# Optimization experiments

Measured on AMD Instinct MI355X. Metric: run time of the kernel, lower is better.

Reference implementation:

```python
import jax, jax.numpy as jnp
import numpy as np

NC = 100000   # n cells
NG = 8000     # n genes
D = 128       # h_dim
E_CG, E_GC, E_CC, E_GG = 1500000, 1500000, 1000000, 200000
SLOPE = 0.05  # LeakyReLU negative slope
LN_EPS = 1e-5


def setup_inputs() -> dict:
    key = jax.random.key(0)
    ks = jax.random.split(key, 16)
    f32 = jnp.float32
    inp = {
        "h_cell": jax.random.normal(ks[0], (NC, D), f32),
        "h_gene": jax.random.normal(ks[1], (NG, D), f32),
        "src_cg": jax.random.randint(ks[2], (E_CG,), 0, NC),
        "dst_cg": jax.random.randint(ks[3], (E_CG,), 0, NG),
        "src_gc": jax.random.randint(ks[4], (E_GC,), 0, NG),
        "dst_gc": jax.random.randint(ks[5], (E_GC,), 0, NC),
        "src_cc": jax.random.randint(ks[6], (E_CC,), 0, NC),
        "dst_cc": jax.random.randint(ks[7], (E_CC,), 0, NC),
        "src_gg": jax.random.randint(ks[8], (E_GG,), 0, NG),
        "dst_gg": jax.random.randint(ks[9], (E_GG,), 0, NG),
        "W_cg": jax.random.normal(ks[10], (D, D), f32) * (1.0 / np.sqrt(D)),
        "W_gc": jax.random.normal(ks[11], (D, D), f32) * (1.0 / np.sqrt(D)),
        "W_cc": jax.random.normal(ks[12], (D, D), f32) * (1.0 / np.sqrt(D)),
        "W_gg": jax.random.normal(ks[13], (D, D), f32) * (1.0 / np.sqrt(D)),
        "b_cell": jnp.zeros((D,), f32),
        "b_gene": jnp.zeros((D,), f32),
        "ln_s_cell": jnp.ones((D,), f32),
        "ln_b_cell": jnp.zeros((D,), f32),
        "ln_s_gene": jnp.ones((D,), f32),
        "ln_b_gene": jnp.zeros((D,), f32),
    }
    return inp


def _rel_conv(h_src, W, src, dst, n_dst):
    # per-relation GraphConv, norm='right': transform, gather, scatter-sum, / in-degree
    m = (h_src @ W)[src]                                   # [E, D]
    agg = jax.ops.segment_sum(m, dst, num_segments=n_dst)  # [n_dst, D]
    deg = jax.ops.segment_sum(jnp.ones(dst.shape, m.dtype), dst, num_segments=n_dst)
    return agg / jnp.clip(deg, 1.0)[:, None]


def _layernorm(x, s, b):
    mu = jnp.mean(x, axis=-1, keepdims=True)
    var = jnp.var(x, axis=-1, keepdims=True)
    return (x - mu) * jax.lax.rsqrt(var + LN_EPS) * s + b


def _leaky(x):
    return jnp.where(x >= 0, x, SLOPE * x)


def _shared_layer(hc, hg, idx, p):
    # aggregate='sum' over relations targeting each dst ntype, then bias, act, LN
    oc = (_rel_conv(hg, p["W_gc"], idx["src_gc"], idx["dst_gc"], NC)
          + _rel_conv(hc, p["W_cc"], idx["src_cc"], idx["dst_cc"], NC)
          + p["b_cell"])
    og = (_rel_conv(hc, p["W_cg"], idx["src_cg"], idx["dst_cg"], NG)
          + _rel_conv(hg, p["W_gg"], idx["src_gg"], idx["dst_gg"], NG)
          + p["b_gene"])
    oc = _layernorm(_leaky(oc), p["ln_s_cell"], p["ln_b_cell"])
    og = _layernorm(_leaky(og), p["ln_s_gene"], p["ln_b_gene"])
    return oc, og


def reference(h_cell, h_gene, src_cg, dst_cg, src_gc, dst_gc, src_cc, dst_cc,
              src_gg, dst_gg, W_cg, W_gc, W_cc, W_gg, b_cell, b_gene,
              ln_s_cell, ln_b_cell, ln_s_gene, ln_b_gene):
    idx = dict(src_cg=src_cg, dst_cg=dst_cg, src_gc=src_gc, dst_gc=dst_gc,
               src_cc=src_cc, dst_cc=dst_cc, src_gg=src_gg, dst_gg=dst_gg)
    p = dict(W_cg=W_cg, W_gc=W_gc, W_cc=W_cc, W_gg=W_gg,
             b_cell=b_cell, b_gene=b_gene,
             ln_s_cell=ln_s_cell, ln_b_cell=ln_b_cell,
             ln_s_gene=ln_s_gene, ln_b_gene=ln_b_gene)
    hc, hg = h_cell, h_gene
    for _ in range(2):  # num_hidden_layers=2, SAME shared layer both times
        hc, hg = _shared_layer(hc, hg, idx, p)
    # pack the heterogeneous output dict as one array: [NC+NG, D]
    return jnp.concatenate([hc, hg], axis=0)
```

## Files before the change

### kernel.cpp

```cpp
#include <hip/hip_runtime.h>

#define NCELL 100000
#define NGENE 8000
#define DIM   128
#define NE_CG 1500000
#define NE_GC 1500000
#define NE_CC 1000000
#define NE_GG 200000
#define SLOPE 0.05f
#define LN_EPS 1e-5f

typedef __attribute__((ext_vector_type(2))) _Float16 f16x2;
typedef __attribute__((ext_vector_type(8))) _Float16 f16x8;
typedef __attribute__((ext_vector_type(4))) float f32x4;

__device__ __forceinline__ unsigned short f2h(float x) {
    return __builtin_bit_cast(unsigned short, (_Float16)x);
}
__device__ __forceinline__ unsigned pack2h(float x, float y) {
    f16x2 h = { (_Float16)x, (_Float16)y };
    return __builtin_bit_cast(unsigned, h);
}
__device__ __forceinline__ f16x2 u2h2(unsigned u) {
    return __builtin_bit_cast(f16x2, u);
}

__global__ __launch_bounds__(256)
void conv2_k(const float* __restrict__ inc, unsigned short* __restrict__ outc,
             const float* __restrict__ ing, unsigned short* __restrict__ outg,
             int cellBlocks, int n2c, int n2g) {
    const float* in; unsigned short* out; int i, n2;
    if ((int)blockIdx.x < cellBlocks) {
        in = inc; out = outc; n2 = n2c; i = blockIdx.x * 256 + threadIdx.x;
    } else {
        in = ing; out = outg; n2 = n2g; i = (blockIdx.x - cellBlocks) * 256 + threadIdx.x;
    }
    if (i < n2) {
        float2 v = ((const float2*)in)[i];
        ((unsigned*)out)[i] = pack2h(v.x, v.y);
    }
}

__global__ void pack2_w_k(const float* __restrict__ WAc, const float* __restrict__ WBc,
                          unsigned short* __restrict__ Wpc,
                          const float* __restrict__ WAg, const float* __restrict__ WBg,
                          unsigned short* __restrict__ Wpg) {
    int bb = blockIdx.x;
    const float *WA, *WB; unsigned short* Wp;
    if (bb < 64) { WA = WAc; WB = WBc; Wp = Wpc; }
    else { bb -= 64; WA = WAg; WB = WBg; Wp = Wpg; }
    int lane = threadIdx.x;
    int t = bb >> 3, c = bb & 7;
    int n = t * 16 + (lane & 15);
    int k0 = c * 32 + (lane >> 4) * 8;
    #pragma unroll
    for (int j = 0; j < 8; ++j) {
        int k = k0 + j;
        float x = (k < 128) ? WA[k * 128 + n] : WB[(k - 128) * 128 + n];
        Wp[((size_t)(bb * 64 + lane)) * 8 + j] = f2h(x);
    }
}

struct RelP {
    const int* src; const int* dst; int n; int shift;
    int nbins; int N; int cap;
    int* deg; int* offg; int* bkt;
    int* bcur; unsigned* stg;
    int cblk0;
    int sblk0;
};

__global__ __launch_bounds__(256)
void bin_fill4_k(RelP r0, RelP r1, RelP r2, RelP r3) {
    int b = blockIdx.x;
    RelP R = (b >= r3.cblk0) ? r3 : (b >= r2.cblk0) ? r2 : (b >= r1.cblk0) ? r1 : r0;
    int lb = b - R.cblk0;
    __shared__ int cnt[512];
    __shared__ int basem[512];
    int tid = threadIdx.x;
    cnt[tid] = 0; cnt[tid + 256] = 0;
    __syncthreads();
    int base = lb * 4096;
    int bins[16]; int ranks[16]; unsigned pk[16];
    #pragma unroll
    for (int it = 0; it < 16; ++it) {
        int i = base + it * 256 + tid;
        bins[it] = -1;
        if (i < R.n) {
            int d = R.dst[i];
            int bn = d >> R.shift;
            int dl = d & ((1 << R.shift) - 1);
            bins[it] = bn;
            pk[it] = (unsigned)R.src[i] | ((unsigned)dl << 20);
            ranks[it] = atomicAdd(&cnt[bn], 1);
        }
    }
    __syncthreads();
    if (cnt[tid])       basem[tid]       = atomicAdd(&R.bcur[tid],       cnt[tid]);
    if (cnt[tid + 256]) basem[tid + 256] = atomicAdd(&R.bcur[tid + 256], cnt[tid + 256]);
    __syncthreads();
    #pragma unroll
    for (int it = 0; it < 16; ++it)
        if (bins[it] >= 0) {
            int r = basem[bins[it]] + ranks[it];
            if (r >= R.cap) r = R.cap - 1;
            R.stg[(size_t)bins[it] * R.cap + r] = pk[it];
        }
}

__global__ __launch_bounds__(256)
void bin_csr4_k(RelP r0, RelP r1, RelP r2, RelP r3) {
    int b = blockIdx.x;
    RelP R = (b >= r3.sblk0) ? r3 : (b >= r2.sblk0) ? r2 : (b >= r1.sblk0) ? r1 : r0;
    int lb = b - R.sblk0;
    int tid = threadIdx.x;
    int ebase = lb * R.cap;
    int cnt = R.bcur[lb]; if (cnt > R.cap) cnt = R.cap;
    __shared__ int degm[256];
    __shared__ int sc[256];
    __shared__ int cur[256];
    __shared__ int bktl[4352];
    degm[tid] = 0;
    __syncthreads();
    for (int i = tid; i < cnt; i += 256)
        atomicAdd(&degm[(R.stg[ebase + i] >> 20) & 255], 1);
    __syncthreads();
    int x = degm[tid];
    sc[tid] = x;
    __syncthreads();
    for (int ofs = 1; ofs < 256; ofs <<= 1) {
        int t = (tid >= ofs) ? sc[tid - ofs] : 0;
        __syncthreads();
        sc[tid] += t;
        __syncthreads();
    }
    int excl = sc[tid] - x;
    cur[tid] = excl;
    int node = (lb << R.shift) + tid;
    if (tid < (1 << R.shift) && node < R.N) { R.deg[node] = x; R.offg[node] = ebase + excl; }
    __syncthreads();
    for (int i = tid; i < cnt; i += 256) {
        unsigned p = R.stg[ebase + i];
        int dl = (p >> 20) & 255;
        int r = atomicAdd(&cur[dl], 1);
        bktl[r] = (int)(p & 0xFFFFFu);
    }
    __syncthreads();
    for (int i = tid; i < cnt; i += 256)
        R.bkt[ebase + i] = bktl[i];
}

__global__ __launch_bounds__(256)
void gather2_k(const unsigned short* __restrict__ hc, const unsigned short* __restrict__ hg,
               const int* __restrict__ off_gc, const int* __restrict__ deg_gc, const int* __restrict__ bkt_gc,
               const int* __restrict__ off_cc, const int* __restrict__ deg_cc, const int* __restrict__ bkt_cc,
               const int* __restrict__ off_cg, const int* __restrict__ deg_cg, const int* __restrict__ bkt_cg,
               const int* __restrict__ off_gg, const int* __restrict__ deg_gg, const int* __restrict__ bkt_gg,
               unsigned short* __restrict__ Acat_c, unsigned short* __restrict__ Acat_g,
               int geneBlocks) {
    int wave = threadIdx.x >> 6, lane = threadIdx.x & 63;
    int g = lane >> 4, c = lane & 15;
    const unsigned short *hA, *hB;
    const int *offA, *degA, *bktA, *offB, *degB, *bktB;
    unsigned short* Aout; int node, N;
    if ((int)blockIdx.x < geneBlocks) {
        node = blockIdx.x * 4 + wave; N = NGENE;
        hA = hc; offA = off_cg; degA = deg_cg; bktA = bkt_cg;
        hB = hg; offB = off_gg; degB = deg_gg; bktB = bkt_gg;
        Aout = Acat_g;
    } else {
        node = (blockIdx.x - geneBlocks) * 4 + wave; N = NCELL;
        hA = hg; offA = off_gc; degA = deg_gc; bktA = bkt_gc;
        hB = hc; offB = off_cc; degB = deg_cc; bktB = bkt_cc;
        Aout = Acat_c;
    }
    if (node >= N) return;

    int nA = degA[node], sA = offA[node];
    int nB = degB[node], sB = offB[node];

    f16x2 aA[4], aB[4];
    #pragma unroll
    for (int i = 0; i < 4; ++i) { aA[i] = (f16x2)(_Float16)0; aB[i] = (f16x2)(_Float16)0; }
    int mx = (nA > nB) ? nA : nB;

    for (int j0 = 0; j0 < mx; j0 += 32) {
        int l32 = lane & 31;
        int jj = j0 + l32;
        int iv = 0;
        if (lane < 32) { if (jj < nA) iv = bktA[sA + jj]; }
        else           { if (jj < nB) iv = bktB[sB + jj]; }
        int mA = nA - j0;
        int mB = nB - j0;
        #pragma unroll
        for (int t = 0; t < 8; ++t) {
            int j = t * 4 + g;
            int sidxA = __shfl(iv, j);
            int sidxB = __shfl(iv, 32 + j);
            uint4 vA = *(const uint4*)(hA + (size_t)sidxA * DIM + c * 8);
            uint4 vB = *(const uint4*)(hB + (size_t)sidxB * DIM + c * 8);
            if (j < mA) {
                aA[0] += u2h2(vA.x); aA[1] += u2h2(vA.y);
                aA[2] += u2h2(vA.z); aA[3] += u2h2(vA.w);
            }
            if (j < mB) {
                aB[0] += u2h2(vB.x); aB[1] += u2h2(vB.y);
                aB[2] += u2h2(vB.z); aB[3] += u2h2(vB.w);
            }
        }
    }

    float fA[8], fB[8];
    #pragma unroll
    for (int i = 0; i < 4; ++i) {
        fA[2 * i]     = (float)aA[i][0]; fA[2 * i + 1] = (float)aA[i][1];
        fB[2 * i]     = (float)aB[i][0]; fB[2 * i + 1] = (float)aB[i][1];
    }
    #pragma unroll
    for (int i = 0; i < 8; ++i) {
        fA[i] += __shfl_xor(fA[i], 16); fA[i] += __shfl_xor(fA[i], 32);
        fB[i] += __shfl_xor(fB[i], 16); fB[i] += __shfl_xor(fB[i], 32);
    }
    float invA = 1.0f / fmaxf((float)nA, 1.0f);
    float invB = 1.0f / fmaxf((float)nB, 1.0f);
    uint4* outrow = (uint4*)(Aout + (size_t)node * 256);
    if (g == 0) {
        outrow[c] = make_uint4(pack2h(fA[0] * invA, fA[1] * invA), pack2h(fA[2] * invA, fA[3] * invA),
                               pack2h(fA[4] * invA, fA[5] * invA), pack2h(fA[6] * invA, fA[7] * invA));
    } else if (g == 1) {
        outrow[16 + c] = make_uint4(pack2h(fB[0] * invB, fB[1] * invB), pack2h(fB[2] * invB, fB[3] * invB),
                                    pack2h(fB[4] * invB, fB[5] * invB), pack2h(fB[6] * invB, fB[7] * invB));
    }
}

#define GBM 128
__global__ __launch_bounds__(256, 4)
void gemm2_ln_k(const unsigned short* __restrict__ Acat_c, const unsigned short* __restrict__ Acat_g,
                const unsigned short* __restrict__ Wp_c, const unsigned short* __restrict__ Wp_g,
                const float* __restrict__ bias_c, const float* __restrict__ bias_g,
                const float* __restrict__ ls_c, const float* __restrict__ lb_c,
                const float* __restrict__ ls_g, const float* __restrict__ lb_g,
                unsigned short* __restrict__ outh_c, unsigned short* __restrict__ outh_g,
                float* __restrict__ outf_c, float* __restrict__ outf_g,
                int cellBlocks) {
    const unsigned short *A, *Wp; const float *bias, *lns, *lnb;
    unsigned short* outh; float* outf; int M, mb;
    if ((int)blockIdx.x < cellBlocks) {
        A = Acat_c; Wp = Wp_c; bias = bias_c; lns = ls_c; lnb = lb_c;
        outh = outh_c; outf = outf_c; M = NCELL; mb = blockIdx.x;
    } else {
        A = Acat_g; Wp = Wp_g; bias = bias_g; lns = ls_g; lnb = lb_g;
        outh = outh_g; outf = outf_g; M = NGENE; mb = blockIdx.x - cellBlocks;
    }
    int tid = threadIdx.x;
    int wave = tid >> 6, lane = tid & 63;
    int col0 = lane & 15;
    int kq = lane >> 4;
    int m_base = mb * GBM + wave * 32;

    f32x4 acc[2][8];
    #pragma unroll
    for (int mt = 0; mt < 2; ++mt)
        #pragma unroll
        for (int t = 0; t < 8; ++t) acc[mt][t] = (f32x4){0.f, 0.f, 0.f, 0.f};

    const unsigned short* Ar0 = A + (size_t)(m_base + col0) * 256 + kq * 8;
    const unsigned short* Ar1 = Ar0 + 16 * 256;
    #pragma unroll
    for (int cc = 0; cc < 8; ++cc) {
        f16x8 a0 = *(const f16x8*)(Ar0 + cc * 32);
        f16x8 a1 = *(const f16x8*)(Ar1 + cc * 32);
        #pragma unroll
        for (int t = 0; t < 8; ++t) {
            f16x8 b = *(const f16x8*)(Wp + ((t * 8 + cc) * 64 + lane) * 8);
            acc[0][t] = __builtin_amdgcn_mfma_f32_16x16x32_f16(a0, b, acc[0][t], 0, 0, 0);
            acc[1][t] = __builtin_amdgcn_mfma_f32_16x16x32_f16(a1, b, acc[1][t], 0, 0, 0);
        }
    }

    float bias_r[8], s_r[8], b_r[8];
    #pragma unroll
    for (int t = 0; t < 8; ++t) {
        int col = t * 16 + col0;
        bias_r[t] = bias[col]; s_r[t] = lns[col]; b_r[t] = lnb[col];
    }
    #pragma unroll
    for (int mt = 0; mt < 2; ++mt) {
        #pragma unroll
        for (int r = 0; r < 4; ++r) {
            int row = m_base + mt * 16 + kq * 4 + r;
            float v[8]; float sum = 0.f, sq = 0.f;
            #pragma unroll
            for (int t = 0; t < 8; ++t) {
                float x = acc[mt][t][r] + bias_r[t];
                x = (x >= 0.f) ? x : SLOPE * x;
                v[t] = x; sum += x; sq += x * x;
            }
            #pragma unroll
            for (int ofs = 1; ofs <= 8; ofs <<= 1) {
                sum += __shfl_xor(sum, ofs);
                sq  += __shfl_xor(sq, ofs);
            }
            float mu = sum * (1.0f / 128.0f);
            float var = sq * (1.0f / 128.0f) - mu * mu;
            float rstd = rsqrtf(var + LN_EPS);
            if (row < M) {
                if (outh) {
                    #pragma unroll
                    for (int t = 0; t < 8; ++t)
                        outh[(size_t)row * 128 + t * 16 + col0] =
                            f2h((v[t] - mu) * rstd * s_r[t] + b_r[t]);
                } else {
                    #pragma unroll
                    for (int t = 0; t < 8; ++t)
                        outf[(size_t)row * 128 + t * 16 + col0] =
                            (v[t] - mu) * rstd * s_r[t] + b_r[t];
                }
            }
        }
    }
}

extern "C" void kernel_launch(void* const* d_in, const int* in_sizes, int n_in,
                              void* d_out, int out_size, void* d_ws, size_t ws_size,
                              hipStream_t stream) {
    const float* h_cell = (const float*)d_in[0];
    const float* h_gene = (const float*)d_in[1];
    const int* src_cg = (const int*)d_in[2];
    const int* dst_cg = (const int*)d_in[3];
    const int* src_gc = (const int*)d_in[4];
    const int* dst_gc = (const int*)d_in[5];
    const int* src_cc = (const int*)d_in[6];
    const int* dst_cc = (const int*)d_in[7];
    const int* src_gg = (const int*)d_in[8];
    const int* dst_gg = (const int*)d_in[9];
    const float* W_cg = (const float*)d_in[10];
    const float* W_gc = (const float*)d_in[11];
    const float* W_cc = (const float*)d_in[12];
    const float* W_gg = (const float*)d_in[13];
    const float* b_cell = (const float*)d_in[14];
    const float* b_gene = (const float*)d_in[15];
    const float* ln_s_cell = (const float*)d_in[16];
    const float* ln_b_cell = (const float*)d_in[17];
    const float* ln_s_gene = (const float*)d_in[18];
    const float* ln_b_gene = (const float*)d_in[19];
    float* out = (float*)d_out;

    const int MPC = ((NCELL + GBM - 1) / GBM) * GBM;
    const int MPG = ((NGENE + GBM - 1) / GBM) * GBM;
    const int NB_C = (NCELL + 255) / 256;
    const int NB_G = (NGENE + 15) / 16;
    const int CAP_GC = 4352;
    const int CAP_CC = 3072;
    const int CAP_CG = 3584;
    const int CAP_GG = 768;

    char* wsb = (char*)d_ws;
    size_t off = 0;
    auto alloc = [&](size_t bytes) -> char* {
        char* p = wsb + off;
        off = (off + bytes + 255) & ~(size_t)255;
        return p;
    };
    unsigned short* Acat_c = (unsigned short*)alloc((size_t)MPC * 256 * 2);
    unsigned short* Acat_g = (unsigned short*)alloc((size_t)MPG * 256 * 2);
    unsigned short* hcb0 = (unsigned short*)alloc((size_t)NCELL * DIM * 2);
    unsigned short* hgb0 = (unsigned short*)alloc((size_t)NGENE * DIM * 2);
    unsigned short* hcb1 = (unsigned short*)alloc((size_t)NCELL * DIM * 2);
    unsigned short* hgb1 = (unsigned short*)alloc((size_t)NGENE * DIM * 2);
    unsigned short* Wp_cell = (unsigned short*)alloc(65536);
    unsigned short* Wp_gene = (unsigned short*)alloc(65536);
    int ndeg = 2 * NCELL + 2 * NGENE;
    int* degs = (int*)alloc((size_t)ndeg * 4);
    int* deg_gc = degs;
    int* deg_cc = degs + NCELL;
    int* deg_cg = degs + 2 * NCELL;
    int* deg_gg = degs + 2 * NCELL + NGENE;
    int* offs = (int*)alloc((size_t)ndeg * 4);
    int* off_gc = offs;
    int* off_cc = offs + NCELL;
    int* off_cg = offs + 2 * NCELL;
    int* off_gg = offs + 2 * NCELL + NGENE;
    int* bkt_gc = (int*)alloc((size_t)NB_C * CAP_GC * 4);
    int* bkt_cc = (int*)alloc((size_t)NB_C * CAP_CC * 4);
    int* bkt_cg = (int*)alloc((size_t)NB_G * CAP_CG * 4);
    int* bkt_gg = (int*)alloc((size_t)NB_G * CAP_GG * 4);
    unsigned* stg_gc = (unsigned*)alloc((size_t)NB_C * CAP_GC * 4);
    unsigned* stg_cc = (unsigned*)alloc((size_t)NB_C * CAP_CC * 4);
    unsigned* stg_cg = (unsigned*)alloc((size_t)NB_G * CAP_CG * 4);
    unsigned* stg_gg = (unsigned*)alloc((size_t)NB_G * CAP_GG * 4);
    int* binmem = (int*)alloc(4 * 512 * 4);

    const int n2c = NCELL * DIM / 2, n2g = NGENE * DIM / 2;
    const int convCB = (n2c + 255) / 256;
    const int convGB = (n2g + 255) / 256;
    conv2_k<<<convCB + convGB, 256, 0, stream>>>(h_cell, hcb0, h_gene, hgb0, convCB, n2c, n2g);
    pack2_w_k<<<128, 64, 0, stream>>>(W_gc, W_cc, Wp_cell, W_cg, W_gg, Wp_gene);

    hipMemsetAsync(binmem, 0, 4 * 512 * 4, stream);
    const int nbk_gc = (NE_GC + 4095) / 4096;
    const int nbk_cc = (NE_CC + 4095) / 4096;
    const int nbk_cg = (NE_CG + 4095) / 4096;
    const int nbk_gg = (NE_GG + 4095) / 4096;
    auto mkrel = [&](const int* s, const int* d, int n, int shift, int nbins, int N, int cap,
                     int* deg, int* offg, int* bkt, int* bm, unsigned* stg,
                     int cblk0, int sblk0) {
        RelP r;
        r.src = s; r.dst = d; r.n = n; r.shift = shift; r.nbins = nbins; r.N = N; r.cap = cap;
        r.deg = deg; r.offg = offg; r.bkt = bkt;
        r.bcur = bm; r.stg = stg;
        r.cblk0 = cblk0; r.sblk0 = sblk0;
        return r;
    };
    RelP r0 = mkrel(src_gc, dst_gc, NE_GC, 8, NB_C, NCELL, CAP_GC, deg_gc, off_gc, bkt_gc,
                    binmem + 0 * 512, stg_gc, 0, 0);
    RelP r1 = mkrel(src_cc, dst_cc, NE_CC, 8, NB_C, NCELL, CAP_CC, deg_cc, off_cc, bkt_cc,
                    binmem + 1 * 512, stg_cc, nbk_gc, NB_C);
    RelP r2 = mkrel(src_cg, dst_cg, NE_CG, 4, NB_G, NGENE, CAP_CG, deg_cg, off_cg, bkt_cg,
                    binmem + 2 * 512, stg_cg, nbk_gc + nbk_cc, 2 * NB_C);
    RelP r3 = mkrel(src_gg, dst_gg, NE_GG, 4, NB_G, NGENE, CAP_GG, deg_gg, off_gg, bkt_gg,
                    binmem + 3 * 512, stg_gg, nbk_gc + nbk_cc + nbk_cg, 2 * NB_C + NB_G);
    const int cntBlocks = nbk_gc + nbk_cc + nbk_cg + nbk_gg;
    const int csrBlocks = 2 * NB_C + 2 * NB_G;
    bin_fill4_k<<<cntBlocks, 256, 0, stream>>>(r0, r1, r2, r3);
    bin_csr4_k<<<csrBlocks, 256, 0, stream>>>(r0, r1, r2, r3);

    const int gatherCB = NCELL / 4;
    const int gatherGB = (NGENE + 3) / 4;
    const int gemmCB = MPC / GBM;
    const int gemmGB = MPG / GBM;
    const unsigned short* hc = hcb0;
    const unsigned short* hg = hgb0;
    for (int layer = 0; layer < 2; ++layer) {
        int final_ = (layer == 1);
        gather2_k<<<gatherGB + gatherCB, 256, 0, stream>>>(
            hc, hg,
            off_gc, deg_gc, bkt_gc, off_cc, deg_cc, bkt_cc,
            off_cg, deg_cg, bkt_cg, off_gg, deg_gg, bkt_gg,
            Acat_c, Acat_g, gatherGB);
        gemm2_ln_k<<<gemmCB + gemmGB, 256, 0, stream>>>(
            Acat_c, Acat_g, Wp_cell, Wp_gene, b_cell, b_gene,
            ln_s_cell, ln_b_cell, ln_s_gene, ln_b_gene,
            final_ ? nullptr : hcb1, final_ ? nullptr : hgb1,
            final_ ? out : nullptr, final_ ? out + (size_t)NCELL * DIM : nullptr,
            gemmCB);
        hc = hcb1;
        hg = hgb1;
    }
}
```

Measured before the change: 563.6 us.

## Fuse input conversion and weight packing into bin-fill kernel; mask gather tail

Merges the fp32-to-fp16 feature conversion and weight packing kernels into the edge bin-fill kernel as extra block ranges, cutting two launches and letting the independent work overlap. The gather loop now skips sub-iterations beyond the larger of the two neighbor counts and replaces branchy conditional accumulation with bitmasked adds. This trades slightly larger kernel code and shared-memory allocation for conversion blocks in exchange for fewer launches and less divergence.

```diff
diff --git a/kernel.cpp b/kernel.cpp
--- a/kernel.cpp
+++ b/kernel.cpp
@@ -25,42 +25,6 @@
     return __builtin_bit_cast(f16x2, u);
 }
 
-__global__ __launch_bounds__(256)
-void conv2_k(const float* __restrict__ inc, unsigned short* __restrict__ outc,
-             const float* __restrict__ ing, unsigned short* __restrict__ outg,
-             int cellBlocks, int n2c, int n2g) {
-    const float* in; unsigned short* out; int i, n2;
-    if ((int)blockIdx.x < cellBlocks) {
-        in = inc; out = outc; n2 = n2c; i = blockIdx.x * 256 + threadIdx.x;
-    } else {
-        in = ing; out = outg; n2 = n2g; i = (blockIdx.x - cellBlocks) * 256 + threadIdx.x;
-    }
-    if (i < n2) {
-        float2 v = ((const float2*)in)[i];
-        ((unsigned*)out)[i] = pack2h(v.x, v.y);
-    }
-}
-
-__global__ void pack2_w_k(const float* __restrict__ WAc, const float* __restrict__ WBc,
-                          unsigned short* __restrict__ Wpc,
-                          const float* __restrict__ WAg, const float* __restrict__ WBg,
-                          unsigned short* __restrict__ Wpg) {
-    int bb = blockIdx.x;
-    const float *WA, *WB; unsigned short* Wp;
-    if (bb < 64) { WA = WAc; WB = WBc; Wp = Wpc; }
-    else { bb -= 64; WA = WAg; WB = WBg; Wp = Wpg; }
-    int lane = threadIdx.x;
-    int t = bb >> 3, c = bb & 7;
-    int n = t * 16 + (lane & 15);
-    int k0 = c * 32 + (lane >> 4) * 8;
-    #pragma unroll
-    for (int j = 0; j < 8; ++j) {
-        int k = k0 + j;
-        float x = (k < 128) ? WA[k * 128 + n] : WB[(k - 128) * 128 + n];
-        Wp[((size_t)(bb * 64 + lane)) * 8 + j] = f2h(x);
-    }
-}
-
 struct RelP {
     const int* src; const int* dst; int n; int shift;
     int nbins; int N; int cap;
@@ -71,13 +35,50 @@
 };
 
 __global__ __launch_bounds__(256)
-void bin_fill4_k(RelP r0, RelP r1, RelP r2, RelP r3) {
+void pre_k(RelP r0, RelP r1, RelP r2, RelP r3, int packBase, int convBase, int convCB,
+           const float* __restrict__ h_cell, unsigned short* __restrict__ hcb,
+           const float* __restrict__ h_gene, unsigned short* __restrict__ hgb,
+           int n2c, int n2g,
+           const float* __restrict__ WAc, const float* __restrict__ WBc,
+           unsigned short* __restrict__ Wpc,
+           const float* __restrict__ WAg, const float* __restrict__ WBg,
+           unsigned short* __restrict__ Wpg) {
+    __shared__ int cnt[512];
+    __shared__ int basem[512];
     int b = blockIdx.x;
+    int tid = threadIdx.x;
+
+    if (b >= convBase) {
+        int cb = b - convBase;
+        const float* in; unsigned short* out; int i, n2;
+        if (cb < convCB) { in = h_cell; out = hcb; n2 = n2c; i = cb * 256 + tid; }
+        else             { in = h_gene; out = hgb; n2 = n2g; i = (cb - convCB) * 256 + tid; }
+        if (i < n2) {
+            float2 v = ((const float2*)in)[i];
+            ((unsigned*)out)[i] = pack2h(v.x, v.y);
+        }
+        return;
+    }
+    if (b >= packBase) {
+        int sub = (b - packBase) * 4 + (tid >> 6);
+        int lane = tid & 63;
+        const float *WA, *WB; unsigned short* Wp; int bb;
+        if (sub < 64) { WA = WAc; WB = WBc; Wp = Wpc; bb = sub; }
+        else          { WA = WAg; WB = WBg; Wp = Wpg; bb = sub - 64; }
+        int t = bb >> 3, cc = bb & 7;
+        int n = t * 16 + (lane & 15);
+        int k0 = cc * 32 + (lane >> 4) * 8;
+        #pragma unroll
+        for (int j = 0; j < 8; ++j) {
+            int k = k0 + j;
+            float x = (k < 128) ? WA[k * 128 + n] : WB[(k - 128) * 128 + n];
+            Wp[((size_t)(bb * 64 + lane)) * 8 + j] = f2h(x);
+        }
+        return;
+    }
+
     RelP R = (b >= r3.cblk0) ? r3 : (b >= r2.cblk0) ? r2 : (b >= r1.cblk0) ? r1 : r0;
     int lb = b - R.cblk0;
-    __shared__ int cnt[512];
-    __shared__ int basem[512];
-    int tid = threadIdx.x;
     cnt[tid] = 0; cnt[tid + 256] = 0;
     __syncthreads();
     int base = lb * 4096;
@@ -192,20 +193,21 @@
         else           { if (jj < nB) iv = bktB[sB + jj]; }
         int mA = nA - j0;
         int mB = nB - j0;
+        int mxb = mx - j0;
         #pragma unroll
         for (int t = 0; t < 8; ++t) {
-            int j = t * 4 + g;
-            int sidxA = __shfl(iv, j);
-            int sidxB = __shfl(iv, 32 + j);
-            uint4 vA = *(const uint4*)(hA + (size_t)sidxA * DIM + c * 8);
-            uint4 vB = *(const uint4*)(hB + (size_t)sidxB * DIM + c * 8);
-            if (j < mA) {
-                aA[0] += u2h2(vA.x); aA[1] += u2h2(vA.y);
-                aA[2] += u2h2(vA.z); aA[3] += u2h2(vA.w);
-            }
-            if (j < mB) {
-                aB[0] += u2h2(vB.x); aB[1] += u2h2(vB.y);
-                aB[2] += u2h2(vB.z); aB[3] += u2h2(vB.w);
+            if (t * 4 < mxb) {
+                int j = t * 4 + g;
+                int sidxA = __shfl(iv, j);
+                int sidxB = __shfl(iv, 32 + j);
+                uint4 vA = *(const uint4*)(hA + (size_t)sidxA * DIM + c * 8);
+                uint4 vB = *(const uint4*)(hB + (size_t)sidxB * DIM + c * 8);
+                unsigned mskA = (j < mA) ? 0xFFFFFFFFu : 0u;
+                unsigned mskB = (j < mB) ? 0xFFFFFFFFu : 0u;
+                aA[0] += u2h2(vA.x & mskA); aA[1] += u2h2(vA.y & mskA);
+                aA[2] += u2h2(vA.z & mskA); aA[3] += u2h2(vA.w & mskA);
+                aB[0] += u2h2(vB.x & mskB); aB[1] += u2h2(vB.y & mskB);
+                aB[2] += u2h2(vB.z & mskB); aB[3] += u2h2(vB.w & mskB);
             }
         }
     }
@@ -391,12 +393,6 @@
     unsigned* stg_gg = (unsigned*)alloc((size_t)NB_G * CAP_GG * 4);
     int* binmem = (int*)alloc(4 * 512 * 4);
 
-    const int n2c = NCELL * DIM / 2, n2g = NGENE * DIM / 2;
-    const int convCB = (n2c + 255) / 256;
-    const int convGB = (n2g + 255) / 256;
-    conv2_k<<<convCB + convGB, 256, 0, stream>>>(h_cell, hcb0, h_gene, hgb0, convCB, n2c, n2g);
-    pack2_w_k<<<128, 64, 0, stream>>>(W_gc, W_cc, Wp_cell, W_cg, W_gg, Wp_gene);
-
     hipMemsetAsync(binmem, 0, 4 * 512 * 4, stream);
     const int nbk_gc = (NE_GC + 4095) / 4096;
     const int nbk_cc = (NE_CC + 4095) / 4096;
@@ -420,9 +416,18 @@
                     binmem + 2 * 512, stg_cg, nbk_gc + nbk_cc, 2 * NB_C);
     RelP r3 = mkrel(src_gg, dst_gg, NE_GG, 4, NB_G, NGENE, CAP_GG, deg_gg, off_gg, bkt_gg,
                     binmem + 3 * 512, stg_gg, nbk_gc + nbk_cc + nbk_cg, 2 * NB_C + NB_G);
-    const int cntBlocks = nbk_gc + nbk_cc + nbk_cg + nbk_gg;
+    const int fillBlocks = nbk_gc + nbk_cc + nbk_cg + nbk_gg;
     const int csrBlocks = 2 * NB_C + 2 * NB_G;
-    bin_fill4_k<<<cntBlocks, 256, 0, stream>>>(r0, r1, r2, r3);
+
+    const int n2c = NCELL * DIM / 2, n2g = NGENE * DIM / 2;
+    const int convCB = (n2c + 255) / 256;
+    const int convGB = (n2g + 255) / 256;
+    const int packBase = fillBlocks;
+    const int convBase = fillBlocks + 32;
+    const int preBlocks = convBase + convCB + convGB;
+    pre_k<<<preBlocks, 256, 0, stream>>>(r0, r1, r2, r3, packBase, convBase, convCB,
+                                         h_cell, hcb0, h_gene, hgb0, n2c, n2g,
+                                         W_gc, W_cc, Wp_cell, W_cg, W_gg, Wp_gene);
     bin_csr4_k<<<csrBlocks, 256, 0, stream>>>(r0, r1, r2, r3);
 
     const int gatherCB = NCELL / 4;
```

Measured after the change: 488.3 us. 13.4% less time.
